# Kernel tuning notes

Measured on AMD Instinct MI355X. Metric: run time of the kernel, lower is better.

Reference implementation:

```python
import jax, jax.numpy as jnp
import numpy as np

N_NODES = 100000
N_EDGES = 3200000
IN_DIM = 4
HID = 128
OUT_DIM = 4


def setup_inputs() -> dict:
    key = jax.random.key(0)
    ks = jax.random.split(key, 16)
    x = jax.random.normal(ks[0], (N_NODES, IN_DIM), dtype=jnp.float32)
    edge_index = jax.random.randint(ks[1], (2, N_EDGES), 0, N_NODES, dtype=jnp.int32)
    hidden_mask = jax.random.randint(ks[2], (N_NODES,), 0, 2) > 0
    def glorot(k, shape):
        fan_in, fan_out = shape[0], shape[1]
        s = jnp.sqrt(6.0 / (fan_in + fan_out))
        return jax.random.uniform(k, shape, jnp.float32, -s, s)
    return {
        "x": x,
        "edge_index": edge_index,
        "hidden_mask": hidden_mask,
        "W0": glorot(ks[3], (IN_DIM, HID)), "b0": jnp.zeros((HID,), jnp.float32),
        "res_W": glorot(ks[4], (IN_DIM, HID)), "res_b": jnp.zeros((HID,), jnp.float32),
        "W1": glorot(ks[5], (HID, HID)), "b1": jnp.zeros((HID,), jnp.float32),
        "W2": glorot(ks[6], (HID, HID)), "b2": jnp.zeros((HID,), jnp.float32),
        "fc_W": glorot(ks[7], (HID, OUT_DIM)), "fc_b": jnp.zeros((OUT_DIM,), jnp.float32),
    }


def _gcn_norm(edge_index, num_nodes):
    # add self loops, compute symmetric normalization (PyG GCNConv default)
    loop = jnp.arange(num_nodes, dtype=edge_index.dtype)
    src = jnp.concatenate([edge_index[0], loop])
    dst = jnp.concatenate([edge_index[1], loop])
    deg = jax.ops.segment_sum(jnp.ones_like(dst, dtype=jnp.float32), dst,
                              num_segments=num_nodes)
    dis = jnp.where(deg > 0, jax.lax.rsqrt(deg), 0.0)  # deg^{-1/2}, inf -> 0
    norm = dis[src] * dis[dst]  # [E + N]
    return src, dst, norm


def _gcn_conv(h, W, b, src, dst, norm, num_nodes):
    h = h @ W                       # [N, out]
    msg = h[src] * norm[:, None]    # gather + scale, [E+N, out]
    agg = jax.ops.segment_sum(msg, dst, num_segments=num_nodes)
    return agg + b


def reference(x, edge_index, hidden_mask, W0, b0, res_W, res_b, W1, b1, W2, b2, fc_W, fc_b):
    n = x.shape[0]
    src, dst, norm = _gcn_norm(edge_index, n)
    # mask input features (mask broadcast over 4 feature cols)
    h = jnp.where(hidden_mask[:, None], x, 0.0)
    # layer 0: in_dim != hidden -> linear residual
    out0 = _gcn_conv(h, W0, b0, src, dst, norm, n)
    h = jax.nn.relu(out0 + (h @ res_W + res_b))
    # layers 1,2: identity residual
    h = jax.nn.relu(_gcn_conv(h, W1, b1, src, dst, norm, n) + h)
    h = jax.nn.relu(_gcn_conv(h, W2, b2, src, dst, norm, n) + h)
    x_out = h @ fc_W + fc_b
    return (x_out, hidden_mask)
```

## Files before the change

kernel.cpp:

```cpp
#include <hip/hip_runtime.h>
#include <hip/hip_bf16.h>
#include <stdint.h>

#define HID 128
#define NPART 8
#define NCHUNK 256
#define MCHUNK 4096
#define LBITS 10
#define SBITS 22

__global__ void detect_mask_kernel(const unsigned char* __restrict__ p, int nbytes,
                                   int nfloat, int* __restrict__ flags) {
  int stride = blockDim.x * gridDim.x;
  for (int i = blockIdx.x * blockDim.x + threadIdx.x; i < nbytes; i += stride) {
    if ((i & 3) && p[i] != 0) { atomicOr(&flags[0], 1); break; }
  }
  const float* fp = (const float*)p;
  for (int i = blockIdx.x * blockDim.x + threadIdx.x; i < nfloat; i += stride) {
    float f = fp[i];
    if (!(f == 0.0f || f == 1.0f)) { atomicOr(&flags[1], 1); break; }
  }
}

__global__ void expand_mask_h0(const void* __restrict__ maskp, const float4* __restrict__ x4,
                               const int* __restrict__ flags, const float* __restrict__ dis,
                               float* __restrict__ maskout, float* __restrict__ cvec,
                               float4* __restrict__ h0s, int N) {
  int i = blockIdx.x * blockDim.x + threadIdx.x;
  if (i >= N) return;
  float m;
  if (flags[0] == 0)      m = (((const int*)maskp)[i] != 0) ? 1.f : 0.f;
  else if (flags[1] == 0) m = (((const float*)maskp)[i] != 0.f) ? 1.f : 0.f;
  else                    m = (((const unsigned char*)maskp)[i] != 0) ? 1.f : 0.f;
  maskout[i] = m;
  float4 xv = x4[i];
  float4 h0 = make_float4(m * xv.x, m * xv.y, m * xv.z, m * xv.w);
  float* cv = cvec + (size_t)i * 8;
  cv[4] = h0.x; cv[5] = h0.y; cv[6] = h0.z; cv[7] = h0.w;
  float d = dis[i];
  h0s[i] = make_float4(d * h0.x, d * h0.y, d * h0.z, d * h0.w);
}

__global__ void init_gcur_kernel(int* __restrict__ gcur, int n, int CAPB) {
  int i = blockIdx.x * blockDim.x + threadIdx.x;
  if (i < n) gcur[i] = i * CAPB;
}

__global__ void radixA_kernel(const int* __restrict__ src, const int* __restrict__ dst,
                              int* __restrict__ gcur, uint32_t* __restrict__ bdata,
                              int nbin, int CAPB, int E) {
  __shared__ uint32_t sv[MCHUNK];
  __shared__ uint16_t sb[MCHUNK];
  __shared__ int bcnt[1024], boff[1024], gbase[1024];
  __shared__ int wsum[4];
  int t = threadIdx.x;
  int base = blockIdx.x * MCHUNK;
  int m = E - base; if (m > MCHUNK) m = MCHUNK;
  for (int i = t; i < 1024; i += 256) bcnt[i] = 0;
  __syncthreads();
  uint32_t pk[16]; short bn[16];
#pragma unroll
  for (int j = 0; j < 16; j++) {
    int i = base + t + j * 256;
    if (i < base + m) {
      int d = __builtin_nontemporal_load(&dst[i]);
      int s = __builtin_nontemporal_load(&src[i]);
      int b = d >> LBITS;
      pk[j] = ((uint32_t)(d & ((1 << LBITS) - 1)) << SBITS) | (uint32_t)s;
      bn[j] = (short)b;
      atomicAdd(&bcnt[b], 1);
    } else bn[j] = -1;
  }
  __syncthreads();
  {
    int lane = t & 63, w = t >> 6, i0 = t * 4;
    int v0 = bcnt[i0], v1 = bcnt[i0 + 1], v2 = bcnt[i0 + 2], v3 = bcnt[i0 + 3];
    int ts = v0 + v1 + v2 + v3, sc = ts;
    for (int d = 1; d < 64; d <<= 1) { int x = __shfl_up(sc, d, 64); if (lane >= d) sc += x; }
    if (lane == 63) wsum[w] = sc;
    __syncthreads();
    int wo = 0;
    for (int k = 0; k < w; k++) wo += wsum[k];
    int excl = wo + sc - ts;
    boff[i0] = excl; boff[i0 + 1] = excl + v0;
    boff[i0 + 2] = excl + v0 + v1; boff[i0 + 3] = excl + v0 + v1 + v2;
  }
  __syncthreads();
  for (int i = t; i < nbin; i += 256) {
    int c = bcnt[i];
    gbase[i] = c ? atomicAdd(&gcur[i], c) : 0;
  }
  __syncthreads();
  for (int i = t; i < nbin; i += 256) bcnt[i] = boff[i];
  __syncthreads();
#pragma unroll
  for (int j = 0; j < 16; j++) {
    if (bn[j] >= 0) {
      int p = atomicAdd(&bcnt[bn[j]], 1);
      sv[p] = pk[j];
      sb[p] = (uint16_t)bn[j];
    }
  }
  __syncthreads();
  for (int i = t; i < m; i += 256) {
    int b = sb[i];
    int gp = gbase[b] + (i - boff[b]);
    if (gp < (b + 1) * CAPB) bdata[gp] = sv[i];
  }
}

__global__ void btotB_kernel(const int* __restrict__ gcur, int* __restrict__ btot,
                             int nbin, int CAPB) {
  int b = blockIdx.x * blockDim.x + threadIdx.x;
  if (b < nbin) {
    int c = gcur[b] - b * CAPB;
    btot[b] = (c > CAPB) ? CAPB : c;
  }
}

__global__ void radixB_kernel(const uint32_t* __restrict__ bdata, const int* __restrict__ gcur,
                              const int* __restrict__ bstart, int CAPB,
                              int* __restrict__ off, float* __restrict__ dis,
                              int* __restrict__ csr, int N, int E) {
  __shared__ int cnt[1024], loff[1024];
  __shared__ int wsum[4];
  int b = blockIdx.x, t = threadIdx.x;
  int cb = gcur[b] - b * CAPB; if (cb > CAPB) cb = CAPB;
  int gb = bstart[b];
  const uint32_t* bd = bdata + (size_t)b * CAPB;
  for (int i = t; i < 1024; i += 256) cnt[i] = 0;
  __syncthreads();
  for (int i = t; i < cb; i += 256) atomicAdd(&cnt[bd[i] >> SBITS], 1);
  __syncthreads();
  {
    int lane = t & 63, w = t >> 6, i0 = t * 4;
    int v0 = cnt[i0], v1 = cnt[i0 + 1], v2 = cnt[i0 + 2], v3 = cnt[i0 + 3];
    int ts = v0 + v1 + v2 + v3, sc = ts;
    for (int d = 1; d < 64; d <<= 1) { int x = __shfl_up(sc, d, 64); if (lane >= d) sc += x; }
    if (lane == 63) wsum[w] = sc;
    __syncthreads();
    int wo = 0;
    for (int k = 0; k < w; k++) wo += wsum[k];
    int e0 = wo + sc - ts;
    int e1 = e0 + v0, e2 = e1 + v1, e3 = e2 + v2;
    loff[i0] = e0; loff[i0 + 1] = e1; loff[i0 + 2] = e2; loff[i0 + 3] = e3;
    int d0 = b * 1024 + i0;
    if (d0 + 0 < N) { off[d0 + 0] = gb + e0; dis[d0 + 0] = rsqrtf((float)v0 + 1.0f); }
    if (d0 + 1 < N) { off[d0 + 1] = gb + e1; dis[d0 + 1] = rsqrtf((float)v1 + 1.0f); }
    if (d0 + 2 < N) { off[d0 + 2] = gb + e2; dis[d0 + 2] = rsqrtf((float)v2 + 1.0f); }
    if (d0 + 3 < N) { off[d0 + 3] = gb + e3; dis[d0 + 3] = rsqrtf((float)v3 + 1.0f); }
  }
  if (b == 0 && t == 0) off[N] = E;
  __syncthreads();
  for (int i = t; i < 1024; i += 256) cnt[i] = loff[i];
  __syncthreads();
  for (int i = t; i < cb; i += 256) {
    uint32_t v = bd[i];
    int p = atomicAdd(&cnt[v >> SBITS], 1);
    csr[gb + p] = (int)(v & ((1u << SBITS) - 1));
  }
}

__global__ void scan1_kernel(const int* __restrict__ cnt, int* __restrict__ off,
                             int* __restrict__ bsum, float* __restrict__ dis, int N) {
  __shared__ int wsum[4];
  int t = threadIdx.x, lane = t & 63, w = t >> 6;
  int base = blockIdx.x * 1024 + t * 4;
  int v0 = (base + 0 < N) ? cnt[base + 0] : 0;
  int v1 = (base + 1 < N) ? cnt[base + 1] : 0;
  int v2 = (base + 2 < N) ? cnt[base + 2] : 0;
  int v3 = (base + 3 < N) ? cnt[base + 3] : 0;
  if (dis) {
    if (base + 0 < N) dis[base + 0] = rsqrtf((float)v0 + 1.0f);
    if (base + 1 < N) dis[base + 1] = rsqrtf((float)v1 + 1.0f);
    if (base + 2 < N) dis[base + 2] = rsqrtf((float)v2 + 1.0f);
    if (base + 3 < N) dis[base + 3] = rsqrtf((float)v3 + 1.0f);
  }
  int ts = v0 + v1 + v2 + v3;
  int sc = ts;
  for (int d = 1; d < 64; d <<= 1) {
    int x = __shfl_up(sc, d, 64);
    if (lane >= d) sc += x;
  }
  if (lane == 63) wsum[w] = sc;
  __syncthreads();
  int wo = 0;
  for (int i = 0; i < w; i++) wo += wsum[i];
  int excl = wo + sc - ts;
  if (base + 0 < N) off[base + 0] = excl;
  if (base + 1 < N) off[base + 1] = excl + v0;
  if (base + 2 < N) off[base + 2] = excl + v0 + v1;
  if (base + 3 < N) off[base + 3] = excl + v0 + v1 + v2;
  if (t == 255) bsum[blockIdx.x] = wo + sc;
}

__global__ void scan2_kernel(int* __restrict__ bsum, int nb) {
  if (threadIdx.x == 0 && blockIdx.x == 0) {
    int run = 0;
    for (int i = 0; i < nb; i++) { int v = bsum[i]; bsum[i] = run; run += v; }
  }
}

__global__ void scan3_kernel(int* __restrict__ off, const int* __restrict__ bsum,
                             int* __restrict__ cur, int N, int E) {
  int i = blockIdx.x * blockDim.x + threadIdx.x;
  if (i < N) {
    int o = off[i] + bsum[i >> 10];
    off[i] = o;
    if (cur) cur[i] = o;
  }
  if (i == 0) off[N] = E;
}

__global__ void hist_part_kernel(const int* __restrict__ dst, int* __restrict__ cnt,
                                 int E, int N) {
  int p = blockIdx.x & (NPART - 1);
  int chunk = blockIdx.x >> 3;
  int lo = (int)((long long)p * N / NPART);
  int hi = (int)((long long)(p + 1) * N / NPART);
  int stride = NCHUNK * 256;
  for (int e = chunk * 256 + threadIdx.x; e < E; e += stride) {
    int d = __builtin_nontemporal_load(&dst[e]);
    if (d >= lo && d < hi) atomicAdd(&cnt[d], 1);
  }
}

__global__ void fill_part_kernel(const int* __restrict__ src, const int* __restrict__ dst,
                                 int* __restrict__ cur, int* __restrict__ csr, int E, int N) {
  int p = blockIdx.x & (NPART - 1);
  int chunk = blockIdx.x >> 3;
  int lo = (int)((long long)p * N / NPART);
  int hi = (int)((long long)(p + 1) * N / NPART);
  int stride = NCHUNK * 256;
  for (int e = chunk * 256 + threadIdx.x; e < E; e += stride) {
    int d = __builtin_nontemporal_load(&dst[e]);
    if (d >= lo && d < hi) {
      int s = __builtin_nontemporal_load(&src[e]);
      int pos = atomicAdd(&cur[d], 1);
      csr[pos] = s;
    }
  }
}

__global__ void l0_agg_kernel(const float4* __restrict__ h0s, const float* __restrict__ dis,
                              const int* __restrict__ off, const int* __restrict__ csr,
                              float* __restrict__ cvec, int N) {
  int n = blockIdx.x * blockDim.x + threadIdx.x;
  if (n >= N) return;
  float4 a = h0s[n];
  int e0 = off[n], e1 = off[n + 1];
  int i = e0;
  for (; i + 4 <= e1; i += 4) {
    int s0 = csr[i], s1 = csr[i + 1], s2 = csr[i + 2], s3 = csr[i + 3];
    float4 v0 = h0s[s0], v1 = h0s[s1], v2 = h0s[s2], v3 = h0s[s3];
    a.x += v0.x + v1.x + v2.x + v3.x;
    a.y += v0.y + v1.y + v2.y + v3.y;
    a.z += v0.z + v1.z + v2.z + v3.z;
    a.w += v0.w + v1.w + v2.w + v3.w;
  }
  for (; i < e1; i++) {
    float4 v = h0s[csr[i]];
    a.x += v.x; a.y += v.y; a.z += v.z; a.w += v.w;
  }
  float dn = dis[n];
  float* cv = cvec + (size_t)n * 8;
  cv[0] = dn * a.x; cv[1] = dn * a.y; cv[2] = dn * a.z; cv[3] = dn * a.w;
}

__global__ void l0_combine_kernel(const float* __restrict__ cvec, const float* __restrict__ W0,
                                  const float* __restrict__ b0, const float* __restrict__ resW,
                                  const float* __restrict__ resb, const float* __restrict__ dis,
                                  float* __restrict__ h1, __hip_bfloat16* __restrict__ hbout) {
  int idx = blockIdx.x * blockDim.x + threadIdx.x;
  int n = idx >> 7, c = idx & 127;
  const float* cv = cvec + (size_t)n * 8;
  float acc = b0[c] + resb[c];
#pragma unroll
  for (int k = 0; k < 4; k++) {
    acc += cv[k] * W0[k * HID + c];
    acc += cv[4 + k] * resW[k * HID + c];
  }
  float v = fmaxf(acc, 0.0f);
  h1[idx] = v;
  if (hbout) hbout[idx] = __float2bfloat16(dis[n] * v);
}

__global__ void agg_hid_bf16_kernel(const uint32_t* __restrict__ hb, const float* __restrict__ dis,
                                    const int* __restrict__ off, const int* __restrict__ csr,
                                    float* __restrict__ out, int N) {
  int node = blockIdx.x * 4 + (threadIdx.x >> 6);
  int lane = threadIdx.x & 63;
  if (node >= N) return;
  uint32_t w = hb[(size_t)node * 64 + lane];
  float a0 = __uint_as_float(w << 16);
  float a1 = __uint_as_float(w & 0xffff0000u);
  int e0 = off[node], e1 = off[node + 1];
  int i = e0;
  for (; i + 4 <= e1; i += 4) {
    int s0 = csr[i], s1 = csr[i + 1], s2 = csr[i + 2], s3 = csr[i + 3];
    uint32_t w0 = hb[(size_t)s0 * 64 + lane];
    uint32_t w1 = hb[(size_t)s1 * 64 + lane];
    uint32_t w2 = hb[(size_t)s2 * 64 + lane];
    uint32_t w3 = hb[(size_t)s3 * 64 + lane];
    a0 += __uint_as_float(w0 << 16);  a1 += __uint_as_float(w0 & 0xffff0000u);
    a0 += __uint_as_float(w1 << 16);  a1 += __uint_as_float(w1 & 0xffff0000u);
    a0 += __uint_as_float(w2 << 16);  a1 += __uint_as_float(w2 & 0xffff0000u);
    a0 += __uint_as_float(w3 << 16);  a1 += __uint_as_float(w3 & 0xffff0000u);
  }
  for (; i < e1; i++) {
    uint32_t ww = hb[(size_t)csr[i] * 64 + lane];
    a0 += __uint_as_float(ww << 16);
    a1 += __uint_as_float(ww & 0xffff0000u);
  }
  float dn = dis[node];
  *(float2*)&out[(size_t)node * HID + 2 * lane] = make_float2(dn * a0, dn * a1);
}

__global__ void agg_hid_kernel(const float* __restrict__ h, const float* __restrict__ dis,
                               const int* __restrict__ off, const int* __restrict__ csr,
                               float* __restrict__ out, int N) {
  int node = blockIdx.x * 4 + (threadIdx.x >> 6);
  int lane = threadIdx.x & 63;
  if (node >= N) return;
  float dn = dis[node];
  const float* hrow = h + (size_t)node * HID;
  float a0 = dn * hrow[lane];
  float a1 = dn * hrow[lane + 64];
  int e0 = off[node], e1 = off[node + 1];
  for (int i = e0; i < e1; i++) {
    int s = csr[i];
    float d = dis[s];
    const float* hs = h + (size_t)s * HID;
    a0 += d * hs[lane];
    a1 += d * hs[lane + 64];
  }
  out[(size_t)node * HID + lane] = dn * a0;
  out[(size_t)node * HID + lane + 64] = dn * a1;
}

__global__ void gemm_resid_relu_kernel(float* __restrict__ ag, const float* __restrict__ hres,
                                       const float* __restrict__ W, const float* __restrict__ b,
                                       const float* __restrict__ dis,
                                       __hip_bfloat16* __restrict__ hbout, int N) {
  __shared__ float ash[64 * HID];
  int t = threadIdx.x;
  int n0 = blockIdx.x * 64;
  for (int i = t; i < 64 * HID; i += 256) {
    int gn = n0 + (i >> 7);
    ash[i] = (gn < N) ? ag[(size_t)gn * HID + (i & 127)] : 0.0f;
  }
  __syncthreads();
  int tc = t & 31;
  int tn = t >> 5;
  float acc[8][4];
#pragma unroll
  for (int j = 0; j < 8; j++)
#pragma unroll
    for (int q = 0; q < 4; q++) acc[j][q] = 0.0f;

  for (int k = 0; k < HID; k += 4) {
    float4 w0 = *(const float4*)&W[(k + 0) * HID + tc * 4];
    float4 w1 = *(const float4*)&W[(k + 1) * HID + tc * 4];
    float4 w2 = *(const float4*)&W[(k + 2) * HID + tc * 4];
    float4 w3 = *(const float4*)&W[(k + 3) * HID + tc * 4];
#pragma unroll
    for (int j = 0; j < 8; j++) {
      float4 a = *(const float4*)&ash[(tn * 8 + j) * HID + k];
      acc[j][0] += a.x * w0.x + a.y * w1.x + a.z * w2.x + a.w * w3.x;
      acc[j][1] += a.x * w0.y + a.y * w1.y + a.z * w2.y + a.w * w3.y;
      acc[j][2] += a.x * w0.z + a.y * w1.z + a.z * w2.z + a.w * w3.z;
      acc[j][3] += a.x * w0.w + a.y * w1.w + a.z * w2.w + a.w * w3.w;
    }
  }
  float4 bv = *(const float4*)&b[tc * 4];
#pragma unroll
  for (int j = 0; j < 8; j++) {
    int gn = n0 + tn * 8 + j;
    if (gn < N) {
      float4 hv = *(const float4*)&hres[(size_t)gn * HID + tc * 4];
      float4 o;
      o.x = fmaxf(acc[j][0] + bv.x + hv.x, 0.0f);
      o.y = fmaxf(acc[j][1] + bv.y + hv.y, 0.0f);
      o.z = fmaxf(acc[j][2] + bv.z + hv.z, 0.0f);
      o.w = fmaxf(acc[j][3] + bv.w + hv.w, 0.0f);
      *(float4*)&ag[(size_t)gn * HID + tc * 4] = o;
      if (hbout) {
        float dnn = dis[gn];
        __hip_bfloat162 p01 = __float22bfloat162_rn(make_float2(dnn * o.x, dnn * o.y));
        __hip_bfloat162 p23 = __float22bfloat162_rn(make_float2(dnn * o.z, dnn * o.w));
        *(__hip_bfloat162*)&hbout[(size_t)gn * HID + tc * 4] = p01;
        *(__hip_bfloat162*)&hbout[(size_t)gn * HID + tc * 4 + 2] = p23;
      }
    }
  }
}

__global__ void fc_kernel(const float* __restrict__ h3, const float* __restrict__ fcW,
                          const float* __restrict__ fcb, float* __restrict__ out, int N) {
  __shared__ float sh[64 * 130];
  int t = threadIdx.x;
  int n0 = blockIdx.x * 64;
  for (int i = t; i < 64 * HID; i += 256) {
    int n = i >> 7, k = i & 127;
    int gn = n0 + n;
    sh[n * 130 + k] = (gn < N) ? h3[(size_t)gn * HID + k] : 0.0f;
  }
  __syncthreads();
  int nl = t >> 2, j = t & 3;
  float acc = fcb[j];
  for (int k = 0; k < HID; k++) acc += sh[nl * 130 + k] * fcW[k * 4 + j];
  int gn = n0 + nl;
  if (gn < N) out[(size_t)gn * 4 + j] = acc;
}

extern "C" void kernel_launch(void* const* d_in, const int* in_sizes, int n_in,
                              void* d_out, int out_size, void* d_ws, size_t ws_size,
                              hipStream_t stream) {
  const float* x = (const float*)d_in[0];
  const int* edge = (const int*)d_in[1];
  const void* maskp = d_in[2];
  const float* W0 = (const float*)d_in[3];
  const float* b0 = (const float*)d_in[4];
  const float* resW = (const float*)d_in[5];
  const float* resb = (const float*)d_in[6];
  const float* W1 = (const float*)d_in[7];
  const float* b1 = (const float*)d_in[8];
  const float* W2 = (const float*)d_in[9];
  const float* b2 = (const float*)d_in[10];
  const float* fcW = (const float*)d_in[11];
  const float* fcb = (const float*)d_in[12];
  float* out = (float*)d_out;

  int N = in_sizes[0] / 4;
  int E = in_sizes[1] / 2;
  const int* srcp = edge;
  const int* dstp = edge + E;

  char* ws = (char*)d_ws;
  size_t cursor = 0;
  auto alloc = [&](size_t bytes) { char* p = ws + cursor; cursor += (bytes + 511) & ~(size_t)511; return p; };
  int* flags = (int*)alloc(16);
  int* cnt = (int*)alloc((size_t)N * 4);
  float* dis = (float*)alloc((size_t)N * 4);
  int* off = (int*)alloc((size_t)(N + 1) * 4);
  int* bsum = (int*)alloc(1024);
  int nbin = (N + 1023) >> 10;
  int* gcur = (int*)alloc((size_t)(nbin + 1) * 4);
  int* btot = (int*)alloc((size_t)(nbin + 1) * 4);
  int* bstart = (int*)alloc((size_t)(nbin + 1) * 4);
  int* csr = (int*)alloc((size_t)E * 4);
  float* h0s = (float*)alloc((size_t)N * 4 * 4);
  float* cvec = (float*)alloc((size_t)N * 8 * 4);
  float* buf0 = (float*)alloc((size_t)N * HID * 4);
  float* buf1 = (float*)alloc((size_t)N * HID * 4);
  size_t base_cursor = cursor;
  __hip_bfloat16* hb = (__hip_bfloat16*)alloc((size_t)N * HID * 2);
  bool use_bf16 = (cursor <= ws_size);
  if (!use_bf16) {
    hb = nullptr;
    if (base_cursor > ws_size) return;
  }

  long long expect = (long long)E / (nbin > 0 ? nbin : 1);
  int CAPB = (int)((((expect * 5) / 4 + 127) / 64) * 64);
  if (CAPB < 256) CAPB = 256;
  size_t bdata_bytes = (size_t)nbin * CAPB * 4;
  bool use_radix = (N <= (1 << SBITS)) && (nbin <= 1024) &&
                   (bdata_bytes <= (size_t)N * HID * 4);
  uint32_t* bdata = (uint32_t*)buf1;

  int nThreadsN = (N + 255) / 256;

  hipMemsetAsync(flags, 0, 16, stream);
  detect_mask_kernel<<<256, 256, 0, stream>>>((const unsigned char*)maskp, N, N / 4, flags);

  if (use_radix) {
    init_gcur_kernel<<<(nbin + 255) / 256, 256, 0, stream>>>(gcur, nbin, CAPB);
    radixA_kernel<<<(E + MCHUNK - 1) / MCHUNK, 256, 0, stream>>>(srcp, dstp, gcur, bdata,
                                                                 nbin, CAPB, E);
    btotB_kernel<<<(nbin + 255) / 256, 256, 0, stream>>>(gcur, btot, nbin, CAPB);
    scan1_kernel<<<1, 256, 0, stream>>>(btot, bstart, bsum, nullptr, nbin);
    scan2_kernel<<<1, 64, 0, stream>>>(bsum, 1);
    scan3_kernel<<<(nbin + 255) / 256, 256, 0, stream>>>(bstart, bsum, nullptr, nbin, E);
    radixB_kernel<<<nbin, 256, 0, stream>>>(bdata, gcur, bstart, CAPB, off, dis, csr, N, E);
  } else {
    hipMemsetAsync(cnt, 0, (size_t)N * 4, stream);
    int nb = (N + 1023) / 1024;
    hist_part_kernel<<<NPART * NCHUNK, 256, 0, stream>>>(dstp, cnt, E, N);
    scan1_kernel<<<nb, 256, 0, stream>>>(cnt, off, bsum, dis, N);
    scan2_kernel<<<1, 64, 0, stream>>>(bsum, nb);
    scan3_kernel<<<nThreadsN, 256, 0, stream>>>(off, bsum, cnt, N, E);
    fill_part_kernel<<<NPART * NCHUNK, 256, 0, stream>>>(srcp, dstp, cnt, csr, E, N);
  }

  expand_mask_h0<<<nThreadsN, 256, 0, stream>>>(maskp, (const float4*)x, flags, dis,
                                                out + (size_t)N * 4, cvec, (float4*)h0s, N);

  l0_agg_kernel<<<nThreadsN, 256, 0, stream>>>((const float4*)h0s, dis, off, csr, cvec, N);
  l0_combine_kernel<<<(N * HID + 255) / 256, 256, 0, stream>>>(cvec, W0, b0, resW, resb, dis,
                                                               buf0, hb);

  if (use_bf16)
    agg_hid_bf16_kernel<<<(N + 3) / 4, 256, 0, stream>>>((const uint32_t*)hb, dis, off, csr, buf1, N);
  else
    agg_hid_kernel<<<(N + 3) / 4, 256, 0, stream>>>(buf0, dis, off, csr, buf1, N);
  gemm_resid_relu_kernel<<<(N + 63) / 64, 256, 0, stream>>>(buf1, buf0, W1, b1, dis, hb, N);

  if (use_bf16)
    agg_hid_bf16_kernel<<<(N + 3) / 4, 256, 0, stream>>>((const uint32_t*)hb, dis, off, csr, buf0, N);
  else
    agg_hid_kernel<<<(N + 3) / 4, 256, 0, stream>>>(buf1, dis, off, csr, buf0, N);
  gemm_resid_relu_kernel<<<(N + 63) / 64, 256, 0, stream>>>(buf0, buf1, W2, b2, dis, nullptr, N);

  fc_kernel<<<(N + 63) / 64, 256, 0, stream>>>(buf0, fcW, fcb, out, N);
}
```

Baseline: 606.3 us.

## Fuse last GEMM with FC, merge bucket scan kernels, deepen gather unroll

Three separate changes. The final GEMM+residual+ReLU kernel now also applies the FC layer in registers, using wave shuffles to reduce across columns, so the 128-wide hidden buffer no longer has to be written and read back. The four kernels that counted and scanned the radix buckets become one single-block scan kernel, which removes launch overhead. The bf16 neighbor-gather loop is unrolled to 8 edges so more loads are in flight, at the cost of higher register pressure.

```diff
diff --git a/kernel.cpp b/kernel.cpp
--- a/kernel.cpp
+++ b/kernel.cpp
@@ -109,13 +109,33 @@
   }
 }
 
-__global__ void btotB_kernel(const int* __restrict__ gcur, int* __restrict__ btot,
-                             int nbin, int CAPB) {
-  int b = blockIdx.x * blockDim.x + threadIdx.x;
-  if (b < nbin) {
-    int c = gcur[b] - b * CAPB;
-    btot[b] = (c > CAPB) ? CAPB : c;
-  }
+__global__ void bucket_meta_kernel(const int* __restrict__ gcur, int* __restrict__ bstart,
+                                   int nbin, int CAPB) {
+  __shared__ int wsum[4];
+  int t = threadIdx.x, lane = t & 63, w = t >> 6, i0 = t * 4;
+  int v[4];
+#pragma unroll
+  for (int q = 0; q < 4; q++) {
+    int i = i0 + q;
+    int c = 0;
+    if (i < nbin) {
+      c = gcur[i] - i * CAPB;
+      if (c > CAPB) c = CAPB;
+    }
+    v[q] = c;
+  }
+  int ts = v[0] + v[1] + v[2] + v[3], sc = ts;
+  for (int d = 1; d < 64; d <<= 1) { int x = __shfl_up(sc, d, 64); if (lane >= d) sc += x; }
+  if (lane == 63) wsum[w] = sc;
+  __syncthreads();
+  int wo = 0;
+  for (int k = 0; k < w; k++) wo += wsum[k];
+  int excl = wo + sc - ts;
+  int e[4] = {excl, excl + v[0], excl + v[0] + v[1], excl + v[0] + v[1] + v[2]};
+#pragma unroll
+  for (int q = 0; q < 4; q++)
+    if (i0 + q < nbin) bstart[i0 + q] = e[q];
+  if (t == 255) bstart[nbin] = wo + sc;
 }
 
 __global__ void radixB_kernel(const uint32_t* __restrict__ bdata, const int* __restrict__ gcur,
@@ -285,6 +305,7 @@
   if (hbout) hbout[idx] = __float2bfloat16(dis[n] * v);
 }
 
+#define ACC1(W) { a0 += __uint_as_float((W) << 16); a1 += __uint_as_float((W) & 0xffff0000u); }
 __global__ void agg_hid_bf16_kernel(const uint32_t* __restrict__ hb, const float* __restrict__ dis,
                                     const int* __restrict__ off, const int* __restrict__ csr,
                                     float* __restrict__ out, int N) {
@@ -296,21 +317,30 @@
   float a1 = __uint_as_float(w & 0xffff0000u);
   int e0 = off[node], e1 = off[node + 1];
   int i = e0;
+  for (; i + 8 <= e1; i += 8) {
+    int s0 = csr[i],     s1 = csr[i + 1], s2 = csr[i + 2], s3 = csr[i + 3];
+    int s4 = csr[i + 4], s5 = csr[i + 5], s6 = csr[i + 6], s7 = csr[i + 7];
+    uint32_t w0 = hb[(size_t)s0 * 64 + lane];
+    uint32_t w1 = hb[(size_t)s1 * 64 + lane];
+    uint32_t w2 = hb[(size_t)s2 * 64 + lane];
+    uint32_t w3 = hb[(size_t)s3 * 64 + lane];
+    uint32_t w4 = hb[(size_t)s4 * 64 + lane];
+    uint32_t w5 = hb[(size_t)s5 * 64 + lane];
+    uint32_t w6 = hb[(size_t)s6 * 64 + lane];
+    uint32_t w7 = hb[(size_t)s7 * 64 + lane];
+    ACC1(w0) ACC1(w1) ACC1(w2) ACC1(w3) ACC1(w4) ACC1(w5) ACC1(w6) ACC1(w7)
+  }
   for (; i + 4 <= e1; i += 4) {
     int s0 = csr[i], s1 = csr[i + 1], s2 = csr[i + 2], s3 = csr[i + 3];
     uint32_t w0 = hb[(size_t)s0 * 64 + lane];
     uint32_t w1 = hb[(size_t)s1 * 64 + lane];
     uint32_t w2 = hb[(size_t)s2 * 64 + lane];
     uint32_t w3 = hb[(size_t)s3 * 64 + lane];
-    a0 += __uint_as_float(w0 << 16);  a1 += __uint_as_float(w0 & 0xffff0000u);
-    a0 += __uint_as_float(w1 << 16);  a1 += __uint_as_float(w1 & 0xffff0000u);
-    a0 += __uint_as_float(w2 << 16);  a1 += __uint_as_float(w2 & 0xffff0000u);
-    a0 += __uint_as_float(w3 << 16);  a1 += __uint_as_float(w3 & 0xffff0000u);
+    ACC1(w0) ACC1(w1) ACC1(w2) ACC1(w3)
   }
   for (; i < e1; i++) {
     uint32_t ww = hb[(size_t)csr[i] * 64 + lane];
-    a0 += __uint_as_float(ww << 16);
-    a1 += __uint_as_float(ww & 0xffff0000u);
+    ACC1(ww)
   }
   float dn = dis[node];
   *(float2*)&out[(size_t)node * HID + 2 * lane] = make_float2(dn * a0, dn * a1);
@@ -395,22 +425,72 @@
   }
 }
 
-__global__ void fc_kernel(const float* __restrict__ h3, const float* __restrict__ fcW,
-                          const float* __restrict__ fcb, float* __restrict__ out, int N) {
-  __shared__ float sh[64 * 130];
+__global__ void gemm_resid_fc_kernel(const float* __restrict__ ag, const float* __restrict__ hres,
+                                     const float* __restrict__ W, const float* __restrict__ b,
+                                     const float* __restrict__ fcW, const float* __restrict__ fcb,
+                                     float* __restrict__ out, int N) {
+  __shared__ float ash[64 * HID];
   int t = threadIdx.x;
   int n0 = blockIdx.x * 64;
   for (int i = t; i < 64 * HID; i += 256) {
-    int n = i >> 7, k = i & 127;
-    int gn = n0 + n;
-    sh[n * 130 + k] = (gn < N) ? h3[(size_t)gn * HID + k] : 0.0f;
-  }
-  __syncthreads();
-  int nl = t >> 2, j = t & 3;
-  float acc = fcb[j];
-  for (int k = 0; k < HID; k++) acc += sh[nl * 130 + k] * fcW[k * 4 + j];
-  int gn = n0 + nl;
-  if (gn < N) out[(size_t)gn * 4 + j] = acc;
+    int gn = n0 + (i >> 7);
+    ash[i] = (gn < N) ? ag[(size_t)gn * HID + (i & 127)] : 0.0f;
+  }
+  __syncthreads();
+  int tc = t & 31;
+  int tn = t >> 5;
+  float acc[8][4];
+#pragma unroll
+  for (int j = 0; j < 8; j++)
+#pragma unroll
+    for (int q = 0; q < 4; q++) acc[j][q] = 0.0f;
+
+  for (int k = 0; k < HID; k += 4) {
+    float4 w0 = *(const float4*)&W[(k + 0) * HID + tc * 4];
+    float4 w1 = *(const float4*)&W[(k + 1) * HID + tc * 4];
+    float4 w2 = *(const float4*)&W[(k + 2) * HID + tc * 4];
+    float4 w3 = *(const float4*)&W[(k + 3) * HID + tc * 4];
+#pragma unroll
+    for (int j = 0; j < 8; j++) {
+      float4 a = *(const float4*)&ash[(tn * 8 + j) * HID + k];
+      acc[j][0] += a.x * w0.x + a.y * w1.x + a.z * w2.x + a.w * w3.x;
+      acc[j][1] += a.x * w0.y + a.y * w1.y + a.z * w2.y + a.w * w3.y;
+      acc[j][2] += a.x * w0.z + a.y * w1.z + a.z * w2.z + a.w * w3.z;
+      acc[j][3] += a.x * w0.w + a.y * w1.w + a.z * w2.w + a.w * w3.w;
+    }
+  }
+  float4 f0 = *(const float4*)&fcW[(tc * 4 + 0) * 4];
+  float4 f1 = *(const float4*)&fcW[(tc * 4 + 1) * 4];
+  float4 f2 = *(const float4*)&fcW[(tc * 4 + 2) * 4];
+  float4 f3 = *(const float4*)&fcW[(tc * 4 + 3) * 4];
+  float4 bv = *(const float4*)&b[tc * 4];
+  float4 fb = *(const float4*)&fcb[0];
+#pragma unroll
+  for (int j = 0; j < 8; j++) {
+    int gn = n0 + tn * 8 + j;
+    float4 o = make_float4(0.f, 0.f, 0.f, 0.f);
+    if (gn < N) {
+      float4 hv = *(const float4*)&hres[(size_t)gn * HID + tc * 4];
+      o.x = fmaxf(acc[j][0] + bv.x + hv.x, 0.0f);
+      o.y = fmaxf(acc[j][1] + bv.y + hv.y, 0.0f);
+      o.z = fmaxf(acc[j][2] + bv.z + hv.z, 0.0f);
+      o.w = fmaxf(acc[j][3] + bv.w + hv.w, 0.0f);
+    }
+    float r0 = o.x * f0.x + o.y * f1.x + o.z * f2.x + o.w * f3.x;
+    float r1 = o.x * f0.y + o.y * f1.y + o.z * f2.y + o.w * f3.y;
+    float r2 = o.x * f0.z + o.y * f1.z + o.z * f2.z + o.w * f3.z;
+    float r3 = o.x * f0.w + o.y * f1.w + o.z * f2.w + o.w * f3.w;
+#pragma unroll
+    for (int d = 1; d < 32; d <<= 1) {
+      r0 += __shfl_xor(r0, d, 64);
+      r1 += __shfl_xor(r1, d, 64);
+      r2 += __shfl_xor(r2, d, 64);
+      r3 += __shfl_xor(r3, d, 64);
+    }
+    if (tc == 0 && gn < N)
+      *(float4*)&out[(size_t)gn * 4] =
+          make_float4(r0 + fb.x, r1 + fb.y, r2 + fb.z, r3 + fb.w);
+  }
 }
 
 extern "C" void kernel_launch(void* const* d_in, const int* in_sizes, int n_in,
@@ -446,7 +526,6 @@
   int* bsum = (int*)alloc(1024);
   int nbin = (N + 1023) >> 10;
   int* gcur = (int*)alloc((size_t)(nbin + 1) * 4);
-  int* btot = (int*)alloc((size_t)(nbin + 1) * 4);
   int* bstart = (int*)alloc((size_t)(nbin + 1) * 4);
   int* csr = (int*)alloc((size_t)E * 4);
   float* h0s = (float*)alloc((size_t)N * 4 * 4);
@@ -478,10 +557,7 @@
     init_gcur_kernel<<<(nbin + 255) / 256, 256, 0, stream>>>(gcur, nbin, CAPB);
     radixA_kernel<<<(E + MCHUNK - 1) / MCHUNK, 256, 0, stream>>>(srcp, dstp, gcur, bdata,
                                                                  nbin, CAPB, E);
-    btotB_kernel<<<(nbin + 255) / 256, 256, 0, stream>>>(gcur, btot, nbin, CAPB);
-    scan1_kernel<<<1, 256, 0, stream>>>(btot, bstart, bsum, nullptr, nbin);
-    scan2_kernel<<<1, 64, 0, stream>>>(bsum, 1);
-    scan3_kernel<<<(nbin + 255) / 256, 256, 0, stream>>>(bstart, bsum, nullptr, nbin, E);
+    bucket_meta_kernel<<<1, 256, 0, stream>>>(gcur, bstart, nbin, CAPB);
     radixB_kernel<<<nbin, 256, 0, stream>>>(bdata, gcur, bstart, CAPB, off, dis, csr, N, E);
   } else {
     hipMemsetAsync(cnt, 0, (size_t)N * 4, stream);
@@ -510,7 +586,5 @@
     agg_hid_bf16_kernel<<<(N + 3) / 4, 256, 0, stream>>>((const uint32_t*)hb, dis, off, csr, buf0, N);
   else
     agg_hid_kernel<<<(N + 3) / 4, 256, 0, stream>>>(buf1, dis, off, csr, buf0, N);
-  gemm_resid_relu_kernel<<<(N + 63) / 64, 256, 0, stream>>>(buf0, buf1, W2, b2, dis, nullptr, N);
-
-  fc_kernel<<<(N + 63) / 64, 256, 0, stream>>>(buf0, fcW, fcb, out, N);
-}
+  gemm_resid_fc_kernel<<<(N + 63) / 64, 256, 0, stream>>>(buf0, buf1, W2, b2, fcW, fcb, out, N);
+}
```

New measurement: 555.6 us. -8.4%, faster.
